# Optimization experiments

Hardware: AMD Instinct MI355X
Metric: run time of the kernel (lower is better)

## Reference

```python
import jax, jax.numpy as jnp
import numpy as np

LN_EPS = 1e-5

def _layer_norm(x, gamma, beta):
    mu = x.mean(-1, keepdims=True)
    var = ((x - mu) ** 2).mean(-1, keepdims=True)
    return (x - mu) * jax.lax.rsqrt(var + LN_EPS) * gamma + beta

def _neg_sq_dist(q, p):
    # q: [B,Qtot,H], p: [B,N,H] -> [B,Qtot,N]
    return -jnp.sum((q[:, :, None, :] - p[:, None, :, :]) ** 2, axis=-1)

def setup_inputs() -> dict:
    key = jax.random.key(0)
    k1, k2 = jax.random.split(key)
    B, N, K, Q, H = 512, 10, 5, 5, 256
    Qtot = N * Q  # na_rate = 0
    return {
        "support": jax.random.normal(k1, (B, N * K, H), dtype=jnp.float32),
        "query": jax.random.normal(k2, (B, Qtot, H), dtype=jnp.float32),
        "ln_gamma": jnp.ones((H,), dtype=jnp.float32),
        "ln_beta": jnp.zeros((H,), dtype=jnp.float32),
        "N": N,
        "K": K,
        "Q": Q,
    }

def reference(support, query, ln_gamma, ln_beta, N, K, Q):
    B, _, H = support.shape
    s = _layer_norm(support, ln_gamma, ln_beta).reshape(B, N, K, H)
    q = _layer_norm(query, ln_gamma, ln_beta)          # [B, Qtot, H]
    Qtot = q.shape[1]

    M = s.mean(axis=2)                                  # [B, N, H] mean prototype
    # --- __rectify__ ---
    Xq = _neg_sq_dist(q, M)                             # [B, Qtot, N]
    Cq = jnp.argmax(Xq, axis=-1)                        # [B, Qtot] nearest proto
    # padded support memory [B, N, K+Qtot, H]
    Xp = jnp.pad(s, ((0, 0), (0, 0), (0, Qtot), (0, 0)))
    b_idx = jnp.arange(B)[:, None]
    q_idx = jnp.arange(Qtot)[None, :]
    # each (b,q) writes a unique slot q+K -> no collisions
    Xp = Xp.at[b_idx, Cq, q_idx + K].set(q)
    counts = jax.nn.one_hot(Cq, N, dtype=jnp.float32).sum(axis=1)  # [B, N]
    Xp_size = (K + counts)[:, :, None]                  # [B, N, 1]

    scores = jnp.einsum("bnsh,bnh->bns", Xp, M)[..., None]  # [B,N,S,1]
    M_cos = jax.nn.softmax(scores, axis=1)              # softmax over N dim
    proto = (M_cos * Xp).sum(axis=-2) / Xp_size          # [B, N, H]
    # --- logits ---
    logits = _neg_sq_dist(q, proto)                     # [B, Qtot, N]
    minn = logits.min(axis=-1, keepdims=True)
    logits = jnp.concatenate([logits, minn - 1.0], axis=-1)  # [B, Qtot, N+1]
    pred = jnp.argmax(logits.reshape(-1, N + 1), axis=1)
    return logits, pred
```

## Files before the change

### kernel.cpp

```cpp
#include <hip/hip_runtime.h>
#include <math.h>

#define LN_EPS 1e-5f

constexpr int Nn  = 10;
constexpr int Kk  = 5;
constexpr int Hh  = 256;
constexpr int QT  = 50;
constexpr int NP1 = 11;

template<int CTRL, int RM>
__device__ __forceinline__ float dpp_term(float x) {
    return __int_as_float(__builtin_amdgcn_update_dpp(
        0, __float_as_int(x), CTRL, RM, 0xf, true));
}
__device__ __forceinline__ float sum16_bcast(float v) {
    v += dpp_term<0xB1,  0xf>(v);
    v += dpp_term<0x4E,  0xf>(v);
    v += dpp_term<0x124, 0xf>(v);
    v += dpp_term<0x128, 0xf>(v);
    return v;
}
__device__ __forceinline__ float sum64_lane63(float v) {
    v += dpp_term<0x111, 0xf>(v);
    v += dpp_term<0x112, 0xf>(v);
    v += dpp_term<0x114, 0xf>(v);
    v += dpp_term<0x118, 0xf>(v);
    v += dpp_term<0x142, 0xa>(v);
    v += dpp_term<0x143, 0xc>(v);
    return v;
}
__device__ __forceinline__ float rdlane(float v, int l) {
    return __int_as_float(__builtin_amdgcn_readlane(__float_as_int(v), l));
}
__device__ __forceinline__ float wave64_sum_bcast(float v) {
    return rdlane(sum64_lane63(v), 63);
}

__device__ __forceinline__ float dot16_ilp4(const float y16[16],
                                            const float* __restrict__ rowbase,
                                            int sub) {
    float p0, p1, p2, p3;
    {
        const float4 v = *reinterpret_cast<const float4*>(rowbase + 0 * 64 + sub * 4);
        p0 = y16[0] * v.x; p0 = fmaf(y16[1], v.y, p0);
        p0 = fmaf(y16[2], v.z, p0); p0 = fmaf(y16[3], v.w, p0);
    }
    {
        const float4 v = *reinterpret_cast<const float4*>(rowbase + 1 * 64 + sub * 4);
        p1 = y16[4] * v.x; p1 = fmaf(y16[5], v.y, p1);
        p1 = fmaf(y16[6], v.z, p1); p1 = fmaf(y16[7], v.w, p1);
    }
    {
        const float4 v = *reinterpret_cast<const float4*>(rowbase + 2 * 64 + sub * 4);
        p2 = y16[8] * v.x; p2 = fmaf(y16[9], v.y, p2);
        p2 = fmaf(y16[10], v.z, p2); p2 = fmaf(y16[11], v.w, p2);
    }
    {
        const float4 v = *reinterpret_cast<const float4*>(rowbase + 3 * 64 + sub * 4);
        p3 = y16[12] * v.x; p3 = fmaf(y16[13], v.y, p3);
        p3 = fmaf(y16[14], v.z, p3); p3 = fmaf(y16[15], v.w, p3);
    }
    return (p0 + p1) + (p2 + p3);
}

__global__ __launch_bounds__(1024, 8) void proto_rectify_fused(
    const float* __restrict__ support, const float* __restrict__ query,
    const float* __restrict__ gamma,   const float* __restrict__ beta,
    float* __restrict__ out, int B)
{
    const int b    = blockIdx.x;
    const int tid  = threadIdx.x;
    const int lane = tid & 63;
    const int wave = tid >> 6;
    const int grp  = tid >> 4;
    const int sub  = tid & 15;

    __shared__ float g_s[Hh], bt_s[Hh];
    __shared__ float M_s[Nn][Hh];
    __shared__ float proto_s[Nn][Hh];
    __shared__ float nM_s[Nn], np_s[Nn];
    __shared__ float ny_s[QT];
    __shared__ float score_s[Nn * Kk];
    __shared__ float wsup_s[Nn * Kk];
    __shared__ float wq_s[QT];
    __shared__ int   cq_s[QT];
    __shared__ float sstat_s[Nn * Kk][2];
    __shared__ float qstat_s[QT][2];
    __shared__ int   cnt_s[Nn];

    const float* supB = support + (size_t)b * (Nn * Kk * Hh);
    const float* qryB = query   + (size_t)b * (QT * Hh);

    if (tid < Hh)          g_s[tid]       = gamma[tid];
    else if (tid < 2 * Hh) bt_s[tid - Hh] = beta[tid - Hh];
    if (tid < Nn)          cnt_s[tid]     = 0;

    if (wave < Nn) {
        const int n = wave;
        const float4 g4 = *reinterpret_cast<const float4*>(gamma + lane * 4);
        const float4 b4 = *reinterpret_cast<const float4*>(beta  + lane * 4);
        const float* rows = supB + (size_t)n * Kk * Hh;

        float y[Kk][4];
#pragma unroll
        for (int k = 0; k < Kk; ++k) {
            const float4 x = *reinterpret_cast<const float4*>(rows + k * Hh + lane * 4);
            float s  = x.x + x.y + x.z + x.w;
            float ss = x.x * x.x + x.y * x.y + x.z * x.z + x.w * x.w;
            s  = wave64_sum_bcast(s);
            ss = wave64_sum_bcast(ss);
            const float mu   = s * (1.0f / (float)Hh);
            const float rstd = rsqrtf(ss * (1.0f / (float)Hh) - mu * mu + LN_EPS);
            if (lane == 0) { sstat_s[n * Kk + k][0] = mu; sstat_s[n * Kk + k][1] = rstd; }
            y[k][0] = (x.x - mu) * rstd * g4.x + b4.x;
            y[k][1] = (x.y - mu) * rstd * g4.y + b4.y;
            y[k][2] = (x.z - mu) * rstd * g4.z + b4.z;
            y[k][3] = (x.w - mu) * rstd * g4.w + b4.w;
        }
        float Mv[4];
#pragma unroll
        for (int i = 0; i < 4; ++i)
            Mv[i] = (y[0][i] + y[1][i] + y[2][i] + y[3][i] + y[4][i]) / 5.0f;
        *reinterpret_cast<float4*>(&M_s[n][lane * 4]) =
            make_float4(Mv[0], Mv[1], Mv[2], Mv[3]);

        float pm = Mv[0] * Mv[0];
        pm = fmaf(Mv[1], Mv[1], pm); pm = fmaf(Mv[2], Mv[2], pm); pm = fmaf(Mv[3], Mv[3], pm);
        pm = sum64_lane63(pm);
        if (lane == 63) nM_s[n] = pm;

#pragma unroll
        for (int k = 0; k < Kk; ++k) {
            float p = y[k][0] * Mv[0];
            p = fmaf(y[k][1], Mv[1], p); p = fmaf(y[k][2], Mv[2], p); p = fmaf(y[k][3], Mv[3], p);
            p = sum64_lane63(p);
            if (lane == 63) score_s[n * Kk + k] = p;
        }
    }
    __syncthreads();

    if (grp < QT) {
        const int q = grp;
        const float* row = qryB + (size_t)q * Hh;
        const float nmv = (lane < Nn) ? nM_s[lane] : 0.f;
        float y16[16];
        float s0 = 0.f, s1 = 0.f, s2 = 0.f, s3 = 0.f;
        float t0 = 0.f, t1 = 0.f, t2 = 0.f, t3 = 0.f;
        {
            const float4 x = *reinterpret_cast<const float4*>(row + 0 * 64 + sub * 4);
            y16[0] = x.x; y16[1] = x.y; y16[2] = x.z; y16[3] = x.w;
            s0 = x.x + x.y + x.z + x.w;
            t0 = fmaf(x.x, x.x, fmaf(x.y, x.y, fmaf(x.z, x.z, x.w * x.w)));
        }
        {
            const float4 x = *reinterpret_cast<const float4*>(row + 1 * 64 + sub * 4);
            y16[4] = x.x; y16[5] = x.y; y16[6] = x.z; y16[7] = x.w;
            s1 = x.x + x.y + x.z + x.w;
            t1 = fmaf(x.x, x.x, fmaf(x.y, x.y, fmaf(x.z, x.z, x.w * x.w)));
        }
        {
            const float4 x = *reinterpret_cast<const float4*>(row + 2 * 64 + sub * 4);
            y16[8] = x.x; y16[9] = x.y; y16[10] = x.z; y16[11] = x.w;
            s2 = x.x + x.y + x.z + x.w;
            t2 = fmaf(x.x, x.x, fmaf(x.y, x.y, fmaf(x.z, x.z, x.w * x.w)));
        }
        {
            const float4 x = *reinterpret_cast<const float4*>(row + 3 * 64 + sub * 4);
            y16[12] = x.x; y16[13] = x.y; y16[14] = x.z; y16[15] = x.w;
            s3 = x.x + x.y + x.z + x.w;
            t3 = fmaf(x.x, x.x, fmaf(x.y, x.y, fmaf(x.z, x.z, x.w * x.w)));
        }
        float s  = sum16_bcast((s0 + s1) + (s2 + s3));
        float ss = sum16_bcast((t0 + t1) + (t2 + t3));
        const float mu   = s * (1.0f / (float)Hh);
        const float rstd = rsqrtf(ss * (1.0f / (float)Hh) - mu * mu + LN_EPS);
        if (sub == 0) { qstat_s[q][0] = mu; qstat_s[q][1] = rstd; }

#pragma unroll
        for (int c = 0; c < 4; ++c) {
            const int h = c * 64 + sub * 4;
            const float4 gg = *reinterpret_cast<const float4*>(g_s + h);
            const float4 bb = *reinterpret_cast<const float4*>(bt_s + h);
            y16[c * 4 + 0] = (y16[c * 4 + 0] - mu) * rstd * gg.x + bb.x;
            y16[c * 4 + 1] = (y16[c * 4 + 1] - mu) * rstd * gg.y + bb.y;
            y16[c * 4 + 2] = (y16[c * 4 + 2] - mu) * rstd * gg.z + bb.z;
            y16[c * 4 + 3] = (y16[c * 4 + 3] - mu) * rstd * gg.w + bb.w;
        }
        float n0 = fmaf(y16[0], y16[0], fmaf(y16[1], y16[1],
                   fmaf(y16[2], y16[2], y16[3] * y16[3])));
        float n1 = fmaf(y16[4], y16[4], fmaf(y16[5], y16[5],
                   fmaf(y16[6], y16[6], y16[7] * y16[7])));
        float n2 = fmaf(y16[8], y16[8], fmaf(y16[9], y16[9],
                   fmaf(y16[10], y16[10], y16[11] * y16[11])));
        float n3 = fmaf(y16[12], y16[12], fmaf(y16[13], y16[13],
                   fmaf(y16[14], y16[14], y16[15] * y16[15])));
        float ny = sum16_bcast((n0 + n1) + (n2 + n3));
        if (sub == 0) ny_s[q] = ny;

        float bestd = INFINITY, bestdot = 0.f;
        int bestn = 0;
#pragma unroll
        for (int n = 0; n < Nn; ++n) {
            float p = dot16_ilp4(y16, &M_s[n][0], sub);
            p = sum16_bcast(p);
            const float d = rdlane(nmv, n) - 2.0f * p;
            if (d < bestd) { bestd = d; bestn = n; bestdot = p; }
        }
        if (sub == 0) {
            const float sc  = bestdot;
            const float mx  = fmaxf(sc, 0.f);
            const float e   = expf(sc - mx);
            const float den = e + (float)(Nn - 1) * expf(-mx);
            wq_s[q] = e / den;
            cq_s[q] = bestn;
            atomicAdd(&cnt_s[bestn], 1);
        }
    } else if (grp >= 56 && grp < 56 + Kk && sub == 0) {
        const int k = grp - 56;
        float mx = -INFINITY;
#pragma unroll
        for (int n = 0; n < Nn; ++n) mx = fmaxf(mx, score_s[n * Kk + k]);
        float e[Nn]; float den = 0.f;
#pragma unroll
        for (int n = 0; n < Nn; ++n) { e[n] = expf(score_s[n * Kk + k] - mx); den += e[n]; }
#pragma unroll
        for (int n = 0; n < Nn; ++n) wsup_s[n * Kk + k] = e[n] / den;
    }
    __syncthreads();

    if (wave < Nn) {
        const int n = wave;
        const float4 g4 = *reinterpret_cast<const float4*>(g_s  + lane * 4);
        const float4 b4 = *reinterpret_cast<const float4*>(bt_s + lane * 4);
        const float* rows = supB + (size_t)n * Kk * Hh;

        float acc[4] = {0.f, 0.f, 0.f, 0.f};
#pragma unroll
        for (int k = 0; k < Kk; ++k) {
            const float w    = wsup_s[n * Kk + k];
            const float mu   = sstat_s[n * Kk + k][0];
            const float rstd = sstat_s[n * Kk + k][1];
            const float4 x = *reinterpret_cast<const float4*>(rows + k * Hh + lane * 4);
            acc[0] = fmaf(w, (x.x - mu) * rstd * g4.x + b4.x, acc[0]);
            acc[1] = fmaf(w, (x.y - mu) * rstd * g4.y + b4.y, acc[1]);
            acc[2] = fmaf(w, (x.z - mu) * rstd * g4.z + b4.z, acc[2]);
            acc[3] = fmaf(w, (x.w - mu) * rstd * g4.w + b4.w, acc[3]);
        }
        int myc = -1; float myw = 0.f, mymu = 0.f, myr = 0.f;
        if (lane < QT) {
            myc  = cq_s[lane]; myw = wq_s[lane];
            mymu = qstat_s[lane][0]; myr = qstat_s[lane][1];
        }
        unsigned long long mask = __ballot(lane < QT && myc == n);
        while (mask) {
            const int q = __ffsll(mask) - 1;
            mask &= mask - 1;
            const float w    = rdlane(myw,  q);
            const float mu   = rdlane(mymu, q);
            const float rstd = rdlane(myr,  q);
            const float4 x = *reinterpret_cast<const float4*>(qryB + (size_t)q * Hh + lane * 4);
            acc[0] = fmaf(w, (x.x - mu) * rstd * g4.x + b4.x, acc[0]);
            acc[1] = fmaf(w, (x.y - mu) * rstd * g4.y + b4.y, acc[1]);
            acc[2] = fmaf(w, (x.z - mu) * rstd * g4.z + b4.z, acc[2]);
            acc[3] = fmaf(w, (x.w - mu) * rstd * g4.w + b4.w, acc[3]);
        }
        const float inv = 1.0f / (float)(Kk + cnt_s[n]);
        float pv[4];
#pragma unroll
        for (int i = 0; i < 4; ++i) pv[i] = acc[i] * inv;
        *reinterpret_cast<float4*>(&proto_s[n][lane * 4]) =
            make_float4(pv[0], pv[1], pv[2], pv[3]);
        float pp = pv[0] * pv[0];
        pp = fmaf(pv[1], pv[1], pp); pp = fmaf(pv[2], pv[2], pp); pp = fmaf(pv[3], pv[3], pp);
        pp = sum64_lane63(pp);
        if (lane == 63) np_s[n] = pp;
    }
    __syncthreads();

    if (grp < QT) {
        const int q = grp;
        const float* row  = qryB + (size_t)q * Hh;
        const float  mu   = qstat_s[q][0];
        const float  rstd = qstat_s[q][1];
        const float  npv  = (lane < Nn) ? np_s[lane] : 0.f;
        float y16[16];
#pragma unroll
        for (int c = 0; c < 4; ++c) {
            const int h = c * 64 + sub * 4;
            const float4 x  = *reinterpret_cast<const float4*>(row + h);
            const float4 gg = *reinterpret_cast<const float4*>(g_s + h);
            const float4 bb = *reinterpret_cast<const float4*>(bt_s + h);
            y16[c * 4 + 0] = (x.x - mu) * rstd * gg.x + bb.x;
            y16[c * 4 + 1] = (x.y - mu) * rstd * gg.y + bb.y;
            y16[c * 4 + 2] = (x.z - mu) * rstd * gg.z + bb.z;
            y16[c * 4 + 3] = (x.w - mu) * rstd * gg.w + bb.w;
        }
        const float ny = ny_s[q];

        float mine = 0.f, maxd = -INFINITY, bestd = INFINITY;
        int bestn = 0;
#pragma unroll
        for (int n = 0; n < Nn; ++n) {
            float p = dot16_ilp4(y16, &proto_s[n][0], sub);
            p = sum16_bcast(p);
            const float d = ny + rdlane(npv, n) - 2.0f * p;
            if (sub == n) mine = d;
            maxd = fmaxf(maxd, d);
            if (d < bestd) { bestd = d; bestn = n; }
        }
        float* o = out + ((size_t)b * QT + q) * NP1;
        if (sub < Nn)       o[sub] = -mine;
        else if (sub == Nn) o[Nn]  = -maxd - 1.0f;
        else if (sub == Nn + 1)
            out[(size_t)B * QT * NP1 + (size_t)b * QT + q] = (float)bestn;
    }
}

extern "C" void kernel_launch(void* const* d_in, const int* in_sizes, int n_in,
                              void* d_out, int out_size, void* d_ws, size_t ws_size,
                              hipStream_t stream) {
    const float* support = (const float*)d_in[0];
    const float* query   = (const float*)d_in[1];
    const float* gamma   = (const float*)d_in[2];
    const float* beta    = (const float*)d_in[3];
    float* out = (float*)d_out;

    const int B = in_sizes[0] / (Nn * Kk * Hh);
    proto_rectify_fused<<<B, 1024, 0, stream>>>(support, query, gamma, beta, out, B);
}
```

Baseline: 29.31 us.

## Stage normalized query rows in LDS and overlap query LN with support phase

Query layer norm is now computed once by the six waves left idle during the support phase, and the normalized rows are stored in a shared-memory tile. Later phases (rectify argmin, prototype accumulation, final logits) read that tile instead of reloading queries from global memory and renormalizing them. The mean and prototype buffers are merged into one array, and gamma and beta stay in registers instead of LDS. The cost is a 50x256 float LDS buffer (about 51 KB) per block, which may reduce occupancy.

```diff
diff --git a/kernel.cpp b/kernel.cpp
--- a/kernel.cpp
+++ b/kernel.cpp
@@ -76,9 +76,8 @@
     const int grp  = tid >> 4;
     const int sub  = tid & 15;
 
-    __shared__ float g_s[Hh], bt_s[Hh];
-    __shared__ float M_s[Nn][Hh];
-    __shared__ float proto_s[Nn][Hh];
+    __shared__ float qy_s[QT][Hh];
+    __shared__ float MP_s[Nn][Hh];
     __shared__ float nM_s[Nn], np_s[Nn];
     __shared__ float ny_s[QT];
     __shared__ float score_s[Nn * Kk];
@@ -86,20 +85,17 @@
     __shared__ float wq_s[QT];
     __shared__ int   cq_s[QT];
     __shared__ float sstat_s[Nn * Kk][2];
-    __shared__ float qstat_s[QT][2];
     __shared__ int   cnt_s[Nn];
 
     const float* supB = support + (size_t)b * (Nn * Kk * Hh);
     const float* qryB = query   + (size_t)b * (QT * Hh);
 
-    if (tid < Hh)          g_s[tid]       = gamma[tid];
-    else if (tid < 2 * Hh) bt_s[tid - Hh] = beta[tid - Hh];
-    if (tid < Nn)          cnt_s[tid]     = 0;
-
+    if (tid < Nn) cnt_s[tid] = 0;
+
+    const float4 g4 = *reinterpret_cast<const float4*>(gamma + lane * 4);
+    const float4 b4 = *reinterpret_cast<const float4*>(beta  + lane * 4);
     if (wave < Nn) {
         const int n = wave;
-        const float4 g4 = *reinterpret_cast<const float4*>(gamma + lane * 4);
-        const float4 b4 = *reinterpret_cast<const float4*>(beta  + lane * 4);
         const float* rows = supB + (size_t)n * Kk * Hh;
 
         float y[Kk][4];
@@ -122,7 +118,7 @@
 #pragma unroll
         for (int i = 0; i < 4; ++i)
             Mv[i] = (y[0][i] + y[1][i] + y[2][i] + y[3][i] + y[4][i]) / 5.0f;
-        *reinterpret_cast<float4*>(&M_s[n][lane * 4]) =
+        *reinterpret_cast<float4*>(&MP_s[n][lane * 4]) =
             make_float4(Mv[0], Mv[1], Mv[2], Mv[3]);
 
         float pm = Mv[0] * Mv[0];
@@ -137,72 +133,44 @@
             p = sum64_lane63(p);
             if (lane == 63) score_s[n * Kk + k] = p;
         }
+    } else {
+        for (int r = wave - 10; r < QT; r += 6) {
+            const float4 x = *reinterpret_cast<const float4*>(
+                qryB + (size_t)r * Hh + lane * 4);
+            float s  = x.x + x.y + x.z + x.w;
+            float ss = fmaf(x.x, x.x, fmaf(x.y, x.y, fmaf(x.z, x.z, x.w * x.w)));
+            s  = wave64_sum_bcast(s);
+            ss = wave64_sum_bcast(ss);
+            const float mu   = s * (1.0f / (float)Hh);
+            const float rstd = rsqrtf(ss * (1.0f / (float)Hh) - mu * mu + LN_EPS);
+            float y0 = (x.x - mu) * rstd * g4.x + b4.x;
+            float y1 = (x.y - mu) * rstd * g4.y + b4.y;
+            float y2 = (x.z - mu) * rstd * g4.z + b4.z;
+            float y3 = (x.w - mu) * rstd * g4.w + b4.w;
+            *reinterpret_cast<float4*>(&qy_s[r][lane * 4]) =
+                make_float4(y0, y1, y2, y3);
+            float ny = fmaf(y0, y0, fmaf(y1, y1, fmaf(y2, y2, y3 * y3)));
+            ny = sum64_lane63(ny);
+            if (lane == 63) ny_s[r] = ny;
+        }
     }
     __syncthreads();
 
     if (grp < QT) {
         const int q = grp;
-        const float* row = qryB + (size_t)q * Hh;
         const float nmv = (lane < Nn) ? nM_s[lane] : 0.f;
         float y16[16];
-        float s0 = 0.f, s1 = 0.f, s2 = 0.f, s3 = 0.f;
-        float t0 = 0.f, t1 = 0.f, t2 = 0.f, t3 = 0.f;
-        {
-            const float4 x = *reinterpret_cast<const float4*>(row + 0 * 64 + sub * 4);
-            y16[0] = x.x; y16[1] = x.y; y16[2] = x.z; y16[3] = x.w;
-            s0 = x.x + x.y + x.z + x.w;
-            t0 = fmaf(x.x, x.x, fmaf(x.y, x.y, fmaf(x.z, x.z, x.w * x.w)));
-        }
-        {
-            const float4 x = *reinterpret_cast<const float4*>(row + 1 * 64 + sub * 4);
-            y16[4] = x.x; y16[5] = x.y; y16[6] = x.z; y16[7] = x.w;
-            s1 = x.x + x.y + x.z + x.w;
-            t1 = fmaf(x.x, x.x, fmaf(x.y, x.y, fmaf(x.z, x.z, x.w * x.w)));
-        }
-        {
-            const float4 x = *reinterpret_cast<const float4*>(row + 2 * 64 + sub * 4);
-            y16[8] = x.x; y16[9] = x.y; y16[10] = x.z; y16[11] = x.w;
-            s2 = x.x + x.y + x.z + x.w;
-            t2 = fmaf(x.x, x.x, fmaf(x.y, x.y, fmaf(x.z, x.z, x.w * x.w)));
-        }
-        {
-            const float4 x = *reinterpret_cast<const float4*>(row + 3 * 64 + sub * 4);
-            y16[12] = x.x; y16[13] = x.y; y16[14] = x.z; y16[15] = x.w;
-            s3 = x.x + x.y + x.z + x.w;
-            t3 = fmaf(x.x, x.x, fmaf(x.y, x.y, fmaf(x.z, x.z, x.w * x.w)));
-        }
-        float s  = sum16_bcast((s0 + s1) + (s2 + s3));
-        float ss = sum16_bcast((t0 + t1) + (t2 + t3));
-        const float mu   = s * (1.0f / (float)Hh);
-        const float rstd = rsqrtf(ss * (1.0f / (float)Hh) - mu * mu + LN_EPS);
-        if (sub == 0) { qstat_s[q][0] = mu; qstat_s[q][1] = rstd; }
-
 #pragma unroll
         for (int c = 0; c < 4; ++c) {
-            const int h = c * 64 + sub * 4;
-            const float4 gg = *reinterpret_cast<const float4*>(g_s + h);
-            const float4 bb = *reinterpret_cast<const float4*>(bt_s + h);
-            y16[c * 4 + 0] = (y16[c * 4 + 0] - mu) * rstd * gg.x + bb.x;
-            y16[c * 4 + 1] = (y16[c * 4 + 1] - mu) * rstd * gg.y + bb.y;
-            y16[c * 4 + 2] = (y16[c * 4 + 2] - mu) * rstd * gg.z + bb.z;
-            y16[c * 4 + 3] = (y16[c * 4 + 3] - mu) * rstd * gg.w + bb.w;
-        }
-        float n0 = fmaf(y16[0], y16[0], fmaf(y16[1], y16[1],
-                   fmaf(y16[2], y16[2], y16[3] * y16[3])));
-        float n1 = fmaf(y16[4], y16[4], fmaf(y16[5], y16[5],
-                   fmaf(y16[6], y16[6], y16[7] * y16[7])));
-        float n2 = fmaf(y16[8], y16[8], fmaf(y16[9], y16[9],
-                   fmaf(y16[10], y16[10], y16[11] * y16[11])));
-        float n3 = fmaf(y16[12], y16[12], fmaf(y16[13], y16[13],
-                   fmaf(y16[14], y16[14], y16[15] * y16[15])));
-        float ny = sum16_bcast((n0 + n1) + (n2 + n3));
-        if (sub == 0) ny_s[q] = ny;
-
+            const float4 v = *reinterpret_cast<const float4*>(&qy_s[q][c * 64 + sub * 4]);
+            y16[c * 4 + 0] = v.x; y16[c * 4 + 1] = v.y;
+            y16[c * 4 + 2] = v.z; y16[c * 4 + 3] = v.w;
+        }
         float bestd = INFINITY, bestdot = 0.f;
         int bestn = 0;
 #pragma unroll
         for (int n = 0; n < Nn; ++n) {
-            float p = dot16_ilp4(y16, &M_s[n][0], sub);
+            float p = dot16_ilp4(y16, &MP_s[n][0], sub);
             p = sum16_bcast(p);
             const float d = rdlane(nmv, n) - 2.0f * p;
             if (d < bestd) { bestd = d; bestn = n; bestdot = p; }
@@ -231,8 +199,6 @@
 
     if (wave < Nn) {
         const int n = wave;
-        const float4 g4 = *reinterpret_cast<const float4*>(g_s  + lane * 4);
-        const float4 b4 = *reinterpret_cast<const float4*>(bt_s + lane * 4);
         const float* rows = supB + (size_t)n * Kk * Hh;
 
         float acc[4] = {0.f, 0.f, 0.f, 0.f};
@@ -247,29 +213,24 @@
             acc[2] = fmaf(w, (x.z - mu) * rstd * g4.z + b4.z, acc[2]);
             acc[3] = fmaf(w, (x.w - mu) * rstd * g4.w + b4.w, acc[3]);
         }
-        int myc = -1; float myw = 0.f, mymu = 0.f, myr = 0.f;
-        if (lane < QT) {
-            myc  = cq_s[lane]; myw = wq_s[lane];
-            mymu = qstat_s[lane][0]; myr = qstat_s[lane][1];
-        }
+        int myc = -1; float myw = 0.f;
+        if (lane < QT) { myc = cq_s[lane]; myw = wq_s[lane]; }
         unsigned long long mask = __ballot(lane < QT && myc == n);
         while (mask) {
             const int q = __ffsll(mask) - 1;
             mask &= mask - 1;
-            const float w    = rdlane(myw,  q);
-            const float mu   = rdlane(mymu, q);
-            const float rstd = rdlane(myr,  q);
-            const float4 x = *reinterpret_cast<const float4*>(qryB + (size_t)q * Hh + lane * 4);
-            acc[0] = fmaf(w, (x.x - mu) * rstd * g4.x + b4.x, acc[0]);
-            acc[1] = fmaf(w, (x.y - mu) * rstd * g4.y + b4.y, acc[1]);
-            acc[2] = fmaf(w, (x.z - mu) * rstd * g4.z + b4.z, acc[2]);
-            acc[3] = fmaf(w, (x.w - mu) * rstd * g4.w + b4.w, acc[3]);
+            const float w = rdlane(myw, q);
+            const float4 yv = *reinterpret_cast<const float4*>(&qy_s[q][lane * 4]);
+            acc[0] = fmaf(w, yv.x, acc[0]);
+            acc[1] = fmaf(w, yv.y, acc[1]);
+            acc[2] = fmaf(w, yv.z, acc[2]);
+            acc[3] = fmaf(w, yv.w, acc[3]);
         }
         const float inv = 1.0f / (float)(Kk + cnt_s[n]);
         float pv[4];
 #pragma unroll
         for (int i = 0; i < 4; ++i) pv[i] = acc[i] * inv;
-        *reinterpret_cast<float4*>(&proto_s[n][lane * 4]) =
+        *reinterpret_cast<float4*>(&MP_s[n][lane * 4]) =
             make_float4(pv[0], pv[1], pv[2], pv[3]);
         float pp = pv[0] * pv[0];
         pp = fmaf(pv[1], pv[1], pp); pp = fmaf(pv[2], pv[2], pp); pp = fmaf(pv[3], pv[3], pp);
@@ -280,21 +241,13 @@
 
     if (grp < QT) {
         const int q = grp;
-        const float* row  = qryB + (size_t)q * Hh;
-        const float  mu   = qstat_s[q][0];
-        const float  rstd = qstat_s[q][1];
-        const float  npv  = (lane < Nn) ? np_s[lane] : 0.f;
+        const float npv = (lane < Nn) ? np_s[lane] : 0.f;
         float y16[16];
 #pragma unroll
         for (int c = 0; c < 4; ++c) {
-            const int h = c * 64 + sub * 4;
-            const float4 x  = *reinterpret_cast<const float4*>(row + h);
-            const float4 gg = *reinterpret_cast<const float4*>(g_s + h);
-            const float4 bb = *reinterpret_cast<const float4*>(bt_s + h);
-            y16[c * 4 + 0] = (x.x - mu) * rstd * gg.x + bb.x;
-            y16[c * 4 + 1] = (x.y - mu) * rstd * gg.y + bb.y;
-            y16[c * 4 + 2] = (x.z - mu) * rstd * gg.z + bb.z;
-            y16[c * 4 + 3] = (x.w - mu) * rstd * gg.w + bb.w;
+            const float4 v = *reinterpret_cast<const float4*>(&qy_s[q][c * 64 + sub * 4]);
+            y16[c * 4 + 0] = v.x; y16[c * 4 + 1] = v.y;
+            y16[c * 4 + 2] = v.z; y16[c * 4 + 3] = v.w;
         }
         const float ny = ny_s[q];
 
@@ -302,7 +255,7 @@
         int bestn = 0;
 #pragma unroll
         for (int n = 0; n < Nn; ++n) {
-            float p = dot16_ilp4(y16, &proto_s[n][0], sub);
+            float p = dot16_ilp4(y16, &MP_s[n][0], sub);
             p = sum16_bcast(p);
             const float d = ny + rdlane(npv, n) - 2.0f * p;
             if (sub == n) mine = d;
```

Result: faster. 25.74 us (-12.2%).
